# Kernel optimization log

Measured on AMD Instinct MI355X. Metric: run time of the kernel, lower is better.

Reference implementation:

```python
import jax, jax.numpy as jnp
import numpy as np

NTS = ["User", "Group", "Computer", "Resource", "AIAgent"]
NCNT = [60000, 20000, 40000, 40000, 10000]
FEAT = [22, 6, 14, 5, 9]
# (src_nt_idx, dst_nt_idx) for the 7 active relations:
# User-MemberOf->Group, Group-MemberOf->Group, User-AdminTo->Computer,
# User-ActuallyAccessed->Resource, Computer-LSASSAccessible->Computer,
# AIAgent-AgentCanAccess->Resource, User-GenericAll->User
REL = [(0, 1), (1, 1), (0, 2), (0, 3), (2, 2), (4, 3), (0, 0)]
H, NH, L = 128, 4, 3
HD = H // NH
R = len(REL)
E = 40000


def _forward(xs, Wins, b_in, Wq, Wk, Wv, Wmsg, bmsg, rel_imp, Wo, bo, ln_g, ln_b,
             Wr1, br1, Wr2, br2, We1, be1, We2, be2, edge_index, edge_weight, theta):
    elu = jax.nn.elu
    # input projections + ELU
    h = [elu(x @ W + b_in[i]) for i, (x, W) in enumerate(zip(xs, Wins))]
    # differentiable control suppression: higher theta -> lower edge weight
    ew = edge_weight * (1.0 - jax.nn.sigmoid(theta))[:, None]  # [R, E]
    scale = HD ** -0.5
    for l in range(L):
        agg = [[] for _ in NTS]
        imps = [[] for _ in NTS]
        for r, (si, di) in enumerate(REL):
            src, dst = edge_index[r, 0], edge_index[r, 1]
            nd = h[di].shape[0]
            q = (h[di][dst] @ Wq[l, r]).reshape(-1, NH, HD)
            k = (h[si][src] @ Wk[l, r]).reshape(-1, NH, HD)
            v = (h[si][src] @ Wv[l, r]).reshape(-1, NH, HD)
            s = (q * k).sum(-1) * scale * ew[r][:, None]          # [E, NH]
            m = jax.ops.segment_max(s, dst, num_segments=nd)       # per-dst max
            ex = jnp.exp(s - m[dst])
            z = jax.ops.segment_sum(ex, dst, num_segments=nd)
            p = ex / (z[dst] + 1e-10)                              # neighborhood softmax
            msg = (v * p[..., None]).reshape(-1, H) @ Wmsg[l, r] + bmsg[l, r]
            rw = jax.nn.sigmoid(rel_imp[l, r])
            agg[di].append(jax.ops.segment_sum(msg * rw, dst, num_segments=nd))
            imps[di].append(rw)
        nh = []
        for i in range(len(NTS)):
            if agg[i]:
                w = jax.nn.softmax(jax.lax.stop_gradient(jnp.stack(imps[i])))
                comb = jnp.einsum('r,rnh->nh', w, jnp.stack(agg[i]))
                y = h[i] + comb @ Wo[l, i] + bo[l, i]
                mu = y.mean(-1, keepdims=True)
                var = ((y - mu) ** 2).mean(-1, keepdims=True)
                nh.append((y - mu) / jnp.sqrt(var + 1e-5) * ln_g[l, i] + ln_b[l, i])
            else:
                nh.append(h[i])
        h = [elu(y) for y in nh]
    risks = tuple(jax.nn.sigmoid(elu(hi @ Wr1 + br1) @ Wr2 + br2) for hi in h)
    eps = []
    for r, (si, di) in enumerate(REL):
        comb = jnp.concatenate([h[si][edge_index[r, 0]], h[di][edge_index[r, 1]]], -1)
        eps.append(jax.nn.sigmoid(elu(comb @ We1 + be1) @ We2 + be2))
    return risks + tuple(eps)


def setup_inputs() -> dict:
    key = jax.random.key(0)
    ks = iter(jax.random.split(key, 64))
    d = {}
    for nt, n, f in zip(NTS, NCNT, FEAT):
        d["x_" + nt] = jax.random.normal(next(ks), (n, f), jnp.float32)
    ei = []
    for si, di in REL:
        src = jax.random.randint(next(ks), (E,), 0, NCNT[si])
        dst = jax.random.randint(next(ks), (E,), 0, NCNT[di])
        ei.append(jnp.stack([src, dst]))
    d["edge_index"] = jnp.stack(ei).astype(jnp.int32)
    d["edge_weight"] = jax.random.uniform(next(ks), (R, E), jnp.float32)
    d["theta"] = jax.random.normal(next(ks), (R,), jnp.float32)

    def lin(k, i, o):
        return jax.random.normal(k, (i, o), jnp.float32) / float(np.sqrt(i))

    for nt, f in zip(NTS, FEAT):
        d["Win_" + nt] = lin(next(ks), f, H)
    d["b_in"] = jnp.zeros((len(NTS), H), jnp.float32)
    for nm in ["Wq", "Wk", "Wv", "Wmsg"]:
        d[nm] = jax.random.normal(next(ks), (L, R, H, H), jnp.float32) / float(np.sqrt(H))
    d["bmsg"] = jnp.zeros((L, R, H), jnp.float32)
    d["rel_imp"] = jnp.ones((L, R), jnp.float32)
    d["Wo"] = jax.random.normal(next(ks), (L, len(NTS), H, H), jnp.float32) / float(np.sqrt(H))
    d["bo"] = jnp.zeros((L, len(NTS), H), jnp.float32)
    d["ln_g"] = jnp.ones((L, len(NTS), H), jnp.float32)
    d["ln_b"] = jnp.zeros((L, len(NTS), H), jnp.float32)
    d["Wr1"] = lin(next(ks), H, H // 2)
    d["br1"] = jnp.zeros((H // 2,), jnp.float32)
    d["Wr2"] = lin(next(ks), H // 2, 1)
    d["br2"] = jnp.zeros((1,), jnp.float32)
    d["We1"] = lin(next(ks), 2 * H, H)
    d["be1"] = jnp.zeros((H,), jnp.float32)
    d["We2"] = lin(next(ks), H, 1)
    d["be2"] = jnp.zeros((1,), jnp.float32)
    return d


def reference(x_User, x_Group, x_Computer, x_Resource, x_AIAgent,
              edge_index, edge_weight, theta,
              Win_User, Win_Group, Win_Computer, Win_Resource, Win_AIAgent, b_in,
              Wq, Wk, Wv, Wmsg, bmsg, rel_imp, Wo, bo, ln_g, ln_b,
              Wr1, br1, Wr2, br2, We1, be1, We2, be2):
    xs = [x_User, x_Group, x_Computer, x_Resource, x_AIAgent]
    Wins = [Win_User, Win_Group, Win_Computer, Win_Resource, Win_AIAgent]
    return _forward(xs, Wins, b_in, Wq, Wk, Wv, Wmsg, bmsg, rel_imp, Wo, bo,
                    ln_g, ln_b, Wr1, br1, Wr2, br2, We1, be1, We2, be2,
                    edge_index, edge_weight, theta)
```

## Files before the change

kernel.cpp:

```cpp
#include <hip/hip_runtime.h>

#define CDIV(a,b) (((a)+(b)-1)/(b))
#define EE 40000
#define TOTROWS 170000
#define NDOFF 60001
#define NCHK 59

typedef unsigned short ushort_t;
typedef short bf16x8 __attribute__((ext_vector_type(8)));
typedef float f32x4 __attribute__((ext_vector_type(4)));

__device__ __forceinline__ float eluf(float x) { return x > 0.f ? x : expm1f(x); }
__device__ __forceinline__ float sigf(float x) { return 1.f / (1.f + expf(-x)); }
__device__ __forceinline__ float b2f(ushort_t u) { return __uint_as_float(((unsigned)u) << 16); }
__device__ __forceinline__ ushort_t f2b(float f) {
  unsigned x = __float_as_uint(f);
  x += 0x7FFFu + ((x >> 16) & 1u);
  return (ushort_t)(x >> 16);
}
__device__ __forceinline__ unsigned pk2(float lo, float hi) {
  return (unsigned)f2b(lo) | ((unsigned)f2b(hi) << 16);
}
__device__ __forceinline__ float2 b2f2(unsigned u) {
  return make_float2(__uint_as_float(u << 16), __uint_as_float(u & 0xFFFF0000u));
}

__constant__ const int NDD_C[7] = {20000, 20000, 40000, 40000, 40000, 40000, 60000};

template<int BN>
__device__ __forceinline__ void stage_B(char* Bs, int tid, const ushort_t* Bt, const ushort_t* Bt2) {
#pragma unroll
  for (int i = 0; i < BN / 16; i++) {
    int u = tid + i * 256;
    int nrow = u >> 4;
    const ushort_t* sp = (BN == 256 && u >= 2048) ? (Bt2 + (size_t)(u - 2048) * 8)
                                                  : (Bt + (size_t)u * 8);
    uint4 w = *(const uint4*)sp;
    *(uint4*)(Bs + ((u * 16) ^ ((nrow & 7) << 4))) = w;
  }
}

__device__ __forceinline__ void stage_A_bf16(char* As, int tid, const ushort_t* Ab, int base, int n) {
#pragma unroll
  for (int i = 0; i < 4; i++) {
    int u = tid + i * 256;
    int row = u >> 4;
    int grow = base + row;
    uint4 v = make_uint4(0, 0, 0, 0);
    if (grow < n) v = *(const uint4*)&Ab[(size_t)grow * 128 + (u & 15) * 8];
    *(uint4*)(As + ((u * 16) ^ ((row & 7) << 4))) = v;
  }
}

template<int NF>
__device__ __forceinline__ void mfma_core(const char* As, const char* Bs, int lane, int wcol,
                                          f32x4 (&acc)[4][NF]) {
  int i16 = lane & 15, seg = lane >> 4;
#pragma unroll
  for (int s = 0; s < 4; s++) {
    bf16x8 a[4], b[NF];
#pragma unroll
    for (int m = 0; m < 4; m++) {
      int row = m * 16 + i16;
      a[m] = *(const bf16x8*)(As + ((row * 256 + s * 64 + seg * 16) ^ ((row & 7) << 4)));
    }
#pragma unroll
    for (int nn = 0; nn < NF; nn++) {
      int nr = wcol + nn * 16 + i16;
      b[nn] = *(const bf16x8*)(Bs + ((nr * 256 + s * 64 + seg * 16) ^ ((nr & 7) << 4)));
    }
#pragma unroll
    for (int m = 0; m < 4; m++)
#pragma unroll
      for (int nn = 0; nn < NF; nn++)
        acc[m][nn] = __builtin_amdgcn_mfma_f32_16x16x32_bf16(a[m], b[nn], acc[m][nn], 0, 0, 0);
  }
}

__global__ void prep_scalars(const float* __restrict__ theta, const float* __restrict__ rel_imp,
                             float* __restrict__ scal) {
  int t = threadIdx.x;
  if (t < 7) scal[t] = 1.f - sigf(theta[t]);
  if (t < 21) {
    const int partner[7] = {1, 0, 4, 5, 2, 3, -1};
    int l = t / 7, r = t % 7;
    float rw = sigf(rel_imp[t]);
    float w;
    if (partner[r] < 0) w = 1.f;
    else {
      float rwp = sigf(rel_imp[l * 7 + partner[r]]);
      float e0 = expf(rw), e1 = expf(rwp);
      w = e0 / (e0 + e1);
    }
    scal[8 + t] = w * rw;
  }
}

__global__ __launch_bounds__(256) void transpose_weights(
    const float* __restrict__ Wq, const float* __restrict__ Wk, const float* __restrict__ Wv,
    const float* __restrict__ Wmsg, const float* __restrict__ Wo, const float* __restrict__ We1,
    ushort_t* __restrict__ Wt) {
  int mat = blockIdx.x;
  const float* src;
  if (mat < 21)      src = Wq   + (size_t)mat * 16384;
  else if (mat < 42) src = Wk   + (size_t)(mat - 21) * 16384;
  else if (mat < 63) src = Wv   + (size_t)(mat - 42) * 16384;
  else if (mat < 84) src = Wmsg + (size_t)(mat - 63) * 16384;
  else if (mat < 99) src = Wo   + (size_t)(mat - 84) * 16384;
  else               src = We1  + (size_t)(mat - 99) * 16384;
  __shared__ ushort_t lds[16384];
  int t = threadIdx.x;
  for (int i = 0; i < 64; i++) {
    int u = t + i * 256;
    int k = u >> 7;
    int byte = (u * 2) ^ ((k & 15) << 2);
    *(ushort_t*)((char*)lds + byte) = f2b(src[u]);
  }
  __syncthreads();
  ushort_t* dst = Wt + (size_t)mat * 16384;
  for (int i = 0; i < 64; i++) {
    int u = t + i * 256;
    int n = u >> 7, k = u & 127;
    int byte = ((k * 128 + n) * 2) ^ ((k & 15) << 2);
    dst[u] = *(ushort_t*)((char*)lds + byte);
  }
}

__global__ void transpose_wr1(const float* __restrict__ Wr1, ushort_t* __restrict__ Wt101) {
  int u = blockIdx.x * 256 + threadIdx.x;
  int n = u >> 7, k = u & 127;
  Wt101[u] = f2b(Wr1[k * 64 + n]);
}

template<int F>
__device__ __forceinline__ void inproj_compute(const float* xs, const float* Ws, const float* b2,
                                               ushort_t* hptr, int base, int n, int tid) {
  int cp = tid & 63, rg = tid >> 6;
  float wc0[F], wc1[F];
#pragma unroll
  for (int f = 0; f < F; f++) {
    wc0[f] = Ws[f * 128 + cp * 2];
    wc1[f] = Ws[f * 128 + cp * 2 + 1];
  }
  float bb0 = b2[cp * 2], bb1 = b2[cp * 2 + 1];
  for (int i = 0; i < 16; i++) {
    int row = rg * 16 + i, grow = base + row;
    if (grow >= n) break;
    float a0 = bb0, a1 = bb1;
#pragma unroll
    for (int f = 0; f < F; f++) {
      float xv = xs[row * F + f];
      a0 = fmaf(xv, wc0[f], a0);
      a1 = fmaf(xv, wc1[f], a1);
    }
    *(unsigned*)&hptr[(size_t)grow * 128 + cp * 2] = pk2(eluf(a0), eluf(a1));
  }
}

__global__ __launch_bounds__(256) void in_proj_all(
    const float* __restrict__ x0, const float* __restrict__ x1, const float* __restrict__ x2,
    const float* __restrict__ x3, const float* __restrict__ x4,
    const float* __restrict__ W0, const float* __restrict__ W1, const float* __restrict__ W2,
    const float* __restrict__ W3, const float* __restrict__ W4,
    const float* __restrict__ b_in, ushort_t* __restrict__ h) {
  __shared__ float xs[64 * 22];
  __shared__ float Ws[22 * 128];
  int bb = blockIdx.x, tid = threadIdx.x;
  int ti, lb;
  if (bb < 938)       { ti = 0; lb = bb; }
  else if (bb < 1251) { ti = 1; lb = bb - 938; }
  else if (bb < 1876) { ti = 2; lb = bb - 1251; }
  else if (bb < 2501) { ti = 3; lb = bb - 1876; }
  else                { ti = 4; lb = bb - 2501; }
  const int ROFF_[5] = {0, 60000, 80000, 120000, 160000};
  const int NCNT_[5] = {60000, 20000, 40000, 40000, 10000};
  const int FEAT_[5] = {22, 6, 14, 5, 9};
  const float* xp = (ti == 0) ? x0 : (ti == 1) ? x1 : (ti == 2) ? x2 : (ti == 3) ? x3 : x4;
  const float* Wp = (ti == 0) ? W0 : (ti == 1) ? W1 : (ti == 2) ? W2 : (ti == 3) ? W3 : W4;
  int F = FEAT_[ti], n = NCNT_[ti], base = lb * 64;
  for (int u = tid; u < F * 128; u += 256) Ws[u] = Wp[u];
  for (int u = tid; u < 64 * F; u += 256) {
    int row = u / F, f = u - row * F, grow = base + row;
    xs[u] = (grow < n) ? xp[(size_t)grow * F + f] : 0.f;
  }
  __syncthreads();
  ushort_t* hptr = h + (size_t)ROFF_[ti] * 128;
  const float* b2 = b_in + ti * 128;
  switch (ti) {
    case 0: inproj_compute<22>(xs, Ws, b2, hptr, base, n, tid); break;
    case 1: inproj_compute<6>(xs, Ws, b2, hptr, base, n, tid); break;
    case 2: inproj_compute<14>(xs, Ws, b2, hptr, base, n, tid); break;
    case 3: inproj_compute<5>(xs, Ws, b2, hptr, base, n, tid); break;
    default: inproj_compute<9>(xs, Ws, b2, hptr, base, n, tid); break;
  }
}

__global__ void csr_clear(int* __restrict__ counts) {
  int idx = blockIdx.x * 256 + threadIdx.x;
  if (idx < 7 * NDOFF) counts[idx] = 0;
}

__global__ void csr_hist(const int* __restrict__ ei, int* __restrict__ counts) {
  int idx = blockIdx.x * 256 + threadIdx.x;
  if (idx >= 7 * EE) return;
  int r = idx / EE, e = idx - r * EE;
  int d = ei[(size_t)r * 2 * EE + EE + e];
  atomicAdd(&counts[r * NDOFF + d], 1);
}

__global__ __launch_bounds__(256) void csr_chunk(const int* __restrict__ counts, int* __restrict__ chunkSums) {
  int bb = blockIdx.x;
  int r = bb / NCHK, c = bb - r * NCHK;
  int ndd = NDD_C[r];
  int t = threadIdx.x;
  int v = 0;
#pragma unroll
  for (int j = 0; j < 4; j++) {
    int idx = c * 1024 + t + j * 256;
    if (idx < ndd) v += counts[r * NDOFF + idx];
  }
#pragma unroll
  for (int mm = 32; mm; mm >>= 1) v += __shfl_xor(v, mm);
  __shared__ int ws_[4];
  if ((t & 63) == 0) ws_[t >> 6] = v;
  __syncthreads();
  if (t == 0) chunkSums[bb] = ws_[0] + ws_[1] + ws_[2] + ws_[3];
}

__global__ void csr_chunkscan(const int* __restrict__ chunkSums, int* __restrict__ chunkOffs) {
  int r = threadIdx.x;
  if (r >= 7) return;
  int run = 0;
  for (int c = 0; c < NCHK; c++) {
    chunkOffs[r * NCHK + c] = run;
    run += chunkSums[r * NCHK + c];
  }
}

__global__ __launch_bounds__(1024) void csr_scan_final(
    const int* __restrict__ counts, const int* __restrict__ chunkOffs,
    int* __restrict__ offs, int* __restrict__ cursor) {
  int bb = blockIdx.x;
  int r = bb / NCHK, c = bb - r * NCHK;
  int ndd = NDD_C[r];
  int t = threadIdx.x;
  int idx = c * 1024 + t;
  int v = (idx < ndd) ? counts[r * NDOFF + idx] : 0;
  __shared__ int sc[1024];
  sc[t] = v;
  __syncthreads();
  for (int s = 1; s < 1024; s <<= 1) {
    int add = (t >= s) ? sc[t - s] : 0;
    __syncthreads();
    sc[t] += add;
    __syncthreads();
  }
  if (idx < ndd) {
    int excl = chunkOffs[r * NCHK + c] + sc[t] - v;
    offs[r * NDOFF + idx] = excl;
    cursor[r * NDOFF + idx] = excl;
  }
  if (t == 0 && c == 0) offs[r * NDOFF + ndd] = EE;
}

__global__ void csr_scatter(const int* __restrict__ ei, const float* __restrict__ ew,
                            int* __restrict__ cursor, int* __restrict__ src_csr,
                            float* __restrict__ ew_csr) {
  int idx = blockIdx.x * 256 + threadIdx.x;
  if (idx >= 7 * EE) return;
  int r = idx / EE, e = idx - r * EE;
  int d = ei[(size_t)r * 2 * EE + EE + e];
  int s = ei[(size_t)r * 2 * EE + e];
  int slot = atomicAdd(&cursor[r * NDOFF + d], 1);
  src_csr[r * EE + slot] = s;
  ew_csr[r * EE + slot] = ew[(size_t)r * EE + e];
}

__global__ __launch_bounds__(256) void qkv_proj(
    const ushort_t* __restrict__ hd, const ushort_t* __restrict__ hs,
    const ushort_t* __restrict__ WtQ, const ushort_t* __restrict__ WtK, const ushort_t* __restrict__ WtV,
    ushort_t* __restrict__ Qb, ushort_t* __restrict__ Kb, ushort_t* __restrict__ Vb,
    int ndd, int nds) {
  __shared__ char sm[16384 + 65536];
  char* As = sm;
  char* Bs = sm + 16384;
  int tid = threadIdx.x;
  int nqb = (ndd + 63) >> 6;
  int lane = tid & 63, wv = tid >> 6;
  int i16 = lane & 15, seg = lane >> 4;

  if ((int)blockIdx.x < nqb) {
    int base = blockIdx.x * 64;
    stage_B<128>(Bs, tid, WtQ, nullptr);
    stage_A_bf16(As, tid, hd, base, ndd);
    __syncthreads();
    f32x4 acc[4][2] = {};
    mfma_core<2>(As, Bs, lane, wv * 32, acc);
#pragma unroll
    for (int m = 0; m < 4; m++)
#pragma unroll
      for (int i = 0; i < 4; i++) {
        int grow = base + m * 16 + seg * 4 + i;
        if (grow >= ndd) continue;
#pragma unroll
        for (int nn = 0; nn < 2; nn++) {
          int col = wv * 32 + nn * 16 + i16;
          Qb[(size_t)grow * 128 + col] = f2b(acc[m][nn][i]);
        }
      }
  } else {
    int base = (blockIdx.x - nqb) * 64;
    stage_B<256>(Bs, tid, WtK, WtV);
    stage_A_bf16(As, tid, hs, base, nds);
    __syncthreads();
    f32x4 acc[4][4] = {};
    mfma_core<4>(As, Bs, lane, wv * 64, acc);
#pragma unroll
    for (int m = 0; m < 4; m++)
#pragma unroll
      for (int i = 0; i < 4; i++) {
        int grow = base + m * 16 + seg * 4 + i;
        if (grow >= nds) continue;
#pragma unroll
        for (int nn = 0; nn < 4; nn++) {
          int col = wv * 64 + nn * 16 + i16;
          ushort_t val = f2b(acc[m][nn][i]);
          if (col < 128) Kb[(size_t)grow * 128 + col] = val;
          else           Vb[(size_t)grow * 128 + col - 128] = val;
        }
      }
  }
}

__global__ __launch_bounds__(256) void attn_agg(
    const ushort_t* __restrict__ Qb, const ushort_t* __restrict__ Kb, const ushort_t* __restrict__ Vb,
    const int* __restrict__ offs, const int* __restrict__ src_csr, const float* __restrict__ ew_csr,
    const float* __restrict__ ews, ushort_t* __restrict__ Sb, float* __restrict__ degb, int ndd) {
  int node = blockIdx.x * 4 + (threadIdx.x >> 6);
  if (node >= ndd) return;
  int lane = threadIdx.x & 63;
  int beg = offs[node], end = offs[node + 1];
  float escale = ews[0] * 0.17677669529663687f;
  float q0 = b2f(Qb[(size_t)node * 128 + lane]);
  float q1 = b2f(Qb[(size_t)node * 128 + 64 + lane]);
  float m0 = -3.0e38f, m1 = -3.0e38f, z0 = 0.f, z1 = 0.f, a0 = 0.f, a1 = 0.f;
  for (int p = beg; p < end; p++) {
    int s = src_csr[p];
    float wgt = ew_csr[p] * escale;
    float k0 = b2f(Kb[(size_t)s * 128 + lane]);
    float k1 = b2f(Kb[(size_t)s * 128 + 64 + lane]);
    float p0 = q0 * k0, p1 = q1 * k1;
#pragma unroll
    for (int mm = 16; mm; mm >>= 1) {
      p0 += __shfl_xor(p0, mm);
      p1 += __shfl_xor(p1, mm);
    }
    float s0 = p0 * wgt, s1 = p1 * wgt;
    float nm0 = fmaxf(m0, s0), nm1 = fmaxf(m1, s1);
    float r0 = expf(m0 - nm0), r1 = expf(m1 - nm1);
    float e0 = expf(s0 - nm0), e1 = expf(s1 - nm1);
    float v0 = b2f(Vb[(size_t)s * 128 + lane]);
    float v1 = b2f(Vb[(size_t)s * 128 + 64 + lane]);
    z0 = z0 * r0 + e0; a0 = a0 * r0 + e0 * v0; m0 = nm0;
    z1 = z1 * r1 + e1; a1 = a1 * r1 + e1 * v1; m1 = nm1;
  }
  Sb[(size_t)node * 128 + lane]      = f2b(a0 / (z0 + 1e-10f));
  Sb[(size_t)node * 128 + 64 + lane] = f2b(a1 / (z1 + 1e-10f));
  if (lane == 0) degb[node] = (float)(end - beg);
}

template<int MODE>
__global__ __launch_bounds__(256) void gemm_msg(
    const ushort_t* __restrict__ Ap, const ushort_t* __restrict__ Bt,
    ushort_t* __restrict__ C1, int n,
    const float* __restrict__ coefp, const float* __restrict__ deg, const float* __restrict__ bvec) {
  __shared__ char sm[16384 + 32768];
  char* As = sm;
  char* Bs = sm + 16384;
  int tid = threadIdx.x;
  int base = blockIdx.x * 64;
  stage_B<128>(Bs, tid, Bt, nullptr);
  stage_A_bf16(As, tid, Ap, base, n);
  __syncthreads();
  int lane = tid & 63, wv = tid >> 6;
  int i16 = lane & 15, seg = lane >> 4;
  f32x4 acc[4][2] = {};
  mfma_core<2>(As, Bs, lane, wv * 32, acc);
  float coef = *coefp;
#pragma unroll
  for (int m = 0; m < 4; m++)
#pragma unroll
    for (int i = 0; i < 4; i++) {
      int grow = base + m * 16 + seg * 4 + i;
      if (grow >= n) continue;
      float dg = deg[grow];
#pragma unroll
      for (int nn = 0; nn < 2; nn++) {
        int col = wv * 32 + nn * 16 + i16;
        ushort_t* cp = &C1[(size_t)grow * 128 + col];
        float mv = coef * (acc[m][nn][i] + dg * bvec[col]);
        if (MODE == 1) mv += b2f(*cp);
        *cp = f2b(mv);
      }
    }
}

__global__ __launch_bounds__(256) void gemm_pcat(
    const ushort_t* __restrict__ Ap, const ushort_t* __restrict__ Bt, const ushort_t* __restrict__ Bt2,
    ushort_t* __restrict__ C1, int n) {
  __shared__ char sm[16384 + 65536];
  char* As = sm;
  char* Bs = sm + 16384;
  int tid = threadIdx.x;
  int base = blockIdx.x * 64;
  stage_B<256>(Bs, tid, Bt, Bt2);
  stage_A_bf16(As, tid, Ap, base, n);
  __syncthreads();
  int lane = tid & 63, wv = tid >> 6;
  int i16 = lane & 15, seg = lane >> 4;
  f32x4 acc[4][4] = {};
  mfma_core<4>(As, Bs, lane, wv * 64, acc);
#pragma unroll
  for (int m = 0; m < 4; m++)
#pragma unroll
    for (int i = 0; i < 4; i++) {
      int grow = base + m * 16 + seg * 4 + i;
      if (grow >= n) continue;
#pragma unroll
      for (int nn = 0; nn < 4; nn++) {
        int col = wv * 64 + nn * 16 + i16;
        C1[(size_t)grow * 256 + col] = f2b(acc[m][nn][i]);
      }
    }
}

#define WO_C1 938
#define WO_C2 1251
#define WO_C3 1876
#define WO_C4 2501
#define WO_TOTAL 2814
#define YSTR 132
__global__ __launch_bounds__(256) void wo_ln_all(
    ushort_t* __restrict__ h, const ushort_t* __restrict__ comb, const ushort_t* __restrict__ Wt,
    const float* __restrict__ bo, const float* __restrict__ lng, const float* __restrict__ lnb, int l) {
  int bb = blockIdx.x;
  int tid = threadIdx.x;
  if (bb >= WO_C4) {
    int idx16 = (bb - WO_C4) * 256 + tid;
    if (idx16 >= 80000) return;
    ushort_t* p = h + (size_t)160000 * 128 + (size_t)idx16 * 16;
    uint4 v0 = *(uint4*)p, v1 = *(uint4*)(p + 8);
    unsigned* u0 = (unsigned*)&v0;
    unsigned* u1 = (unsigned*)&v1;
#pragma unroll
    for (int i = 0; i < 4; i++) {
      float2 a = b2f2(u0[i]); u0[i] = pk2(eluf(a.x), eluf(a.y));
      float2 b = b2f2(u1[i]); u1[i] = pk2(eluf(b.x), eluf(b.y));
    }
    *(uint4*)p = v0; *(uint4*)(p + 8) = v1;
    return;
  }
  int ti, lb;
  if (bb < WO_C1)      { ti = 0; lb = bb; }
  else if (bb < WO_C2) { ti = 1; lb = bb - WO_C1; }
  else if (bb < WO_C3) { ti = 2; lb = bb - WO_C2; }
  else                 { ti = 3; lb = bb - WO_C3; }
  const int ROFF_[4] = {0, 60000, 80000, 120000};
  const int NCNT4_[4] = {60000, 20000, 40000, 40000};
  int n = NCNT4_[ti];
  int base = lb * 64;
  int li = l * 5 + ti;
  const ushort_t* A = comb + (size_t)ROFF_[ti] * 128;
  ushort_t* C1 = h + (size_t)ROFF_[ti] * 128;
  const ushort_t* Bt = Wt + (size_t)(84 + li) * 16384;
  const float* bvec = bo + (size_t)li * 128;
  const float* g = lng + (size_t)li * 128;
  const float* b = lnb + (size_t)li * 128;

  __shared__ char sm[16384 + 34048];
  char* As = sm;
  char* Bs = sm + 16384;
  stage_B<128>(Bs, tid, Bt, nullptr);
  stage_A_bf16(As, tid, A, base, n);
  __syncthreads();
  int lane = tid & 63, wv = tid >> 6;
  int i16 = lane & 15, seg = lane >> 4;
  f32x4 acc[4][2] = {};
  mfma_core<2>(As, Bs, lane, wv * 32, acc);

  __syncthreads();
  float* Ys = (float*)sm;
#pragma unroll
  for (int m = 0; m < 4; m++)
#pragma unroll
    for (int i = 0; i < 4; i++) {
      int rl = m * 16 + seg * 4 + i;
      int grow = base + rl;
      if (grow >= n) continue;
#pragma unroll
      for (int nn = 0; nn < 2; nn++) {
        int col = wv * 32 + nn * 16 + i16;
        Ys[rl * YSTR + col] = acc[m][nn][i] + b2f(C1[(size_t)grow * 128 + col]) + bvec[col];
      }
    }
  __syncthreads();
  for (int rr = 0; rr < 16; rr++) {
    int rl = wv * 16 + rr;
    int grow = base + rl;
    if (grow >= n) continue;
    float y0 = Ys[rl * YSTR + lane], y1 = Ys[rl * YSTR + 64 + lane];
    float sum = y0 + y1;
#pragma unroll
    for (int mm = 32; mm; mm >>= 1) sum += __shfl_xor(sum, mm);
    float mu = sum * (1.f / 128.f);
    float d0 = y0 - mu, d1 = y1 - mu;
    float vs = d0 * d0 + d1 * d1;
#pragma unroll
    for (int mm = 32; mm; mm >>= 1) vs += __shfl_xor(vs, mm);
    float rs = rsqrtf(vs * (1.f / 128.f) + 1e-5f);
    C1[(size_t)grow * 128 + lane]      = f2b(eluf(d0 * rs * g[lane] + b[lane]));
    C1[(size_t)grow * 128 + 64 + lane] = f2b(eluf(d1 * rs * g[64 + lane] + b[64 + lane]));
  }
}

__global__ __launch_bounds__(256) void risk_mfma(
    const ushort_t* __restrict__ Hh, const ushort_t* __restrict__ Wt101,
    const float* __restrict__ br1, const float* __restrict__ Wr2, const float* __restrict__ br2,
    float* __restrict__ out) {
  __shared__ char sm[16384 + 16384 + 64 * 68 * 4];
  char* As = sm;
  char* Bs = sm + 16384;
  float* Hs = (float*)(sm + 32768);
  int tid = threadIdx.x;
  int base = blockIdx.x * 64;
#pragma unroll
  for (int i = 0; i < 4; i++) {
    int u = tid + i * 256;
    int nrow = u >> 4;
    uint4 w = *(const uint4*)(Wt101 + (size_t)u * 8);
    *(uint4*)(Bs + ((u * 16) ^ ((nrow & 7) << 4))) = w;
  }
  stage_A_bf16(As, tid, Hh, base, TOTROWS);
  __syncthreads();
  int lane = tid & 63, wv = tid >> 6;
  int i16 = lane & 15, seg = lane >> 4;
  f32x4 acc[4][1] = {};
  mfma_core<1>(As, Bs, lane, wv * 16, acc);
#pragma unroll
  for (int m = 0; m < 4; m++)
#pragma unroll
    for (int i = 0; i < 4; i++) {
      int rl = m * 16 + seg * 4 + i;
      int col = wv * 16 + i16;
      Hs[rl * 68 + col] = eluf(acc[m][0][i] + br1[col]);
    }
  __syncthreads();
  float wr2r = Wr2[lane];
  for (int rr = 0; rr < 16; rr++) {
    int rl = wv * 16 + rr;
    int grow = base + rl;
    float v = Hs[rl * 68 + lane] * wr2r;
#pragma unroll
    for (int mm = 32; mm; mm >>= 1) v += __shfl_xor(v, mm);
    if (lane == 0 && grow < TOTROWS) out[grow] = sigf(v + br2[0]);
  }
}

__global__ __launch_bounds__(256) void edge_combine_all(
    const ushort_t* __restrict__ Pcat, const int* __restrict__ ei,
    const float* __restrict__ be1, const float* __restrict__ We2,
    const float* __restrict__ be2, float* __restrict__ out) {
  const int RSI_[7] = {0, 1, 0, 0, 2, 4, 0};
  const int RDI_[7] = {1, 1, 2, 3, 2, 3, 0};
  const int ROFF_[5] = {0, 60000, 80000, 120000, 160000};
  int bb = blockIdx.x;
  int r = bb / 10000;
  int lane = threadIdx.x & 63;
  int e = (bb % 10000) * 4 + (threadIdx.x >> 6);
  const int* src = ei + (size_t)r * 2 * EE;
  const int* dst = src + EE;
  int s = src[e], d = dst[e];
  const ushort_t* p1 = Pcat + ((size_t)(ROFF_[RSI_[r]] + s)) * 256;
  const ushort_t* p2 = Pcat + ((size_t)(ROFF_[RDI_[r]] + d)) * 256 + 128;
  float h0 = eluf(b2f(p1[lane])      + b2f(p2[lane])      + be1[lane]);
  float h1 = eluf(b2f(p1[64 + lane]) + b2f(p2[64 + lane]) + be1[64 + lane]);
  float v = h0 * We2[lane] + h1 * We2[64 + lane];
#pragma unroll
  for (int mm = 32; mm; mm >>= 1) v += __shfl_xor(v, mm);
  if (lane == 0) out[TOTROWS + (size_t)r * EE + e] = sigf(v + be2[0]);
}

extern "C" void kernel_launch(void* const* d_in, const int* in_sizes, int n_in,
                              void* d_out, int out_size, void* d_ws, size_t ws_size,
                              hipStream_t stream) {
  (void)in_sizes; (void)n_in; (void)out_size;
  static const int NCNT_[5] = {60000, 20000, 40000, 40000, 10000};
  static const int RSI[7] = {0, 1, 0, 0, 2, 4, 0};
  static const int RDI[7] = {1, 1, 2, 3, 2, 3, 0};
  static const int RFIRST[7] = {1, 0, 1, 1, 0, 0, 1};
  static const int ROFF[5] = {0, 60000, 80000, 120000, 160000};

  const float* x[5];    for (int i = 0; i < 5; i++) x[i] = (const float*)d_in[i];
  const int*   ei     = (const int*)d_in[5];
  const float* ew     = (const float*)d_in[6];
  const float* theta  = (const float*)d_in[7];
  const float* Win[5]; for (int i = 0; i < 5; i++) Win[i] = (const float*)d_in[8 + i];
  const float* b_in   = (const float*)d_in[13];
  const float* Wq     = (const float*)d_in[14];
  const float* Wk     = (const float*)d_in[15];
  const float* Wv     = (const float*)d_in[16];
  const float* Wmsg   = (const float*)d_in[17];
  const float* bmsg   = (const float*)d_in[18];
  const float* relimp = (const float*)d_in[19];
  const float* Wo     = (const float*)d_in[20];
  const float* bo     = (const float*)d_in[21];
  const float* lng    = (const float*)d_in[22];
  const float* lnb    = (const float*)d_in[23];
  const float* Wr1    = (const float*)d_in[24];
  const float* br1    = (const float*)d_in[25];
  const float* Wr2    = (const float*)d_in[26];
  const float* br2    = (const float*)d_in[27];
  const float* We1    = (const float*)d_in[28];
  const float* be1    = (const float*)d_in[29];
  const float* We2    = (const float*)d_in[30];
  const float* be2    = (const float*)d_in[31];
  float* out = (float*)d_out;

  char* ws = (char*)d_ws;
  size_t off = 0;
  auto alloc = [&](size_t bytes) -> void* {
    void* p = (void*)(ws + off);
    off = (off + bytes + 255) & ~(size_t)255;
    return p;
  };
  ushort_t* h    = (ushort_t*)alloc((size_t)TOTROWS * 128 * 2);
  ushort_t* comb = (ushort_t*)alloc((size_t)TOTROWS * 128 * 2);
  ushort_t* Qb   = (ushort_t*)alloc((size_t)60000 * 128 * 2);
  ushort_t* Kb   = (ushort_t*)alloc((size_t)60000 * 128 * 2);
  ushort_t* Vb   = (ushort_t*)alloc((size_t)60000 * 128 * 2);
  ushort_t* Sb   = (ushort_t*)alloc((size_t)60000 * 128 * 2);
  float* degb = (float*)alloc((size_t)60000 * 4);
  ushort_t* Wt = (ushort_t*)alloc((size_t)102 * 16384 * 2);
  int* counts  = (int*)alloc((size_t)7 * NDOFF * 4);
  int* cursor  = (int*)alloc((size_t)7 * NDOFF * 4);
  int* offsb   = (int*)alloc((size_t)7 * NDOFF * 4);
  int* src_csr = (int*)alloc((size_t)7 * EE * 4);
  float* ew_csr = (float*)alloc((size_t)7 * EE * 4);
  int* chunkS  = (int*)alloc((size_t)7 * NCHK * 4);
  int* chunkO  = (int*)alloc((size_t)7 * NCHK * 4);
  float* scal = (float*)alloc(256);
  if (off > ws_size) return;
  ushort_t* Pcat = comb;

  prep_scalars<<<1, 64, 0, stream>>>(theta, relimp, scal);
  transpose_weights<<<101, 256, 0, stream>>>(Wq, Wk, Wv, Wmsg, Wo, We1, Wt);
  transpose_wr1<<<32, 256, 0, stream>>>(Wr1, Wt + (size_t)101 * 16384);

  in_proj_all<<<2658, 256, 0, stream>>>(
      x[0], x[1], x[2], x[3], x[4], Win[0], Win[1], Win[2], Win[3], Win[4], b_in, h);

  csr_clear<<<CDIV(7 * NDOFF, 256), 256, 0, stream>>>(counts);
  csr_hist<<<CDIV(7 * EE, 256), 256, 0, stream>>>(ei, counts);
  csr_chunk<<<7 * NCHK, 256, 0, stream>>>(counts, chunkS);
  csr_chunkscan<<<1, 64, 0, stream>>>(chunkS, chunkO);
  csr_scan_final<<<7 * NCHK, 1024, 0, stream>>>(counts, chunkO, offsb, cursor);
  csr_scatter<<<CDIV(7 * EE, 256), 256, 0, stream>>>(ei, ew, cursor, src_csr, ew_csr);

  for (int l = 0; l < 3; l++) {
    for (int r = 0; r < 7; r++) {
      int si = RSI[r], di = RDI[r];
      int nds = NCNT_[si], ndd = NCNT_[di];
      ushort_t* hs = h + (size_t)ROFF[si] * 128;
      ushort_t* hd = h + (size_t)ROFF[di] * 128;
      int lr = l * 7 + r;
      const ushort_t* WtQ = Wt + (size_t)lr * 16384;
      const ushort_t* WtK = Wt + (size_t)(21 + lr) * 16384;
      const ushort_t* WtV = Wt + (size_t)(42 + lr) * 16384;
      const ushort_t* WtM = Wt + (size_t)(63 + lr) * 16384;

      qkv_proj<<<CDIV(ndd, 64) + CDIV(nds, 64), 256, 0, stream>>>(
          hd, hs, WtQ, WtK, WtV, Qb, Kb, Vb, ndd, nds);
      attn_agg<<<CDIV(ndd, 4), 256, 0, stream>>>(
          Qb, Kb, Vb, offsb + (size_t)r * NDOFF, src_csr + (size_t)r * EE,
          ew_csr + (size_t)r * EE, scal + r, Sb, degb, ndd);
      ushort_t* cdst = comb + (size_t)ROFF[di] * 128;
      if (RFIRST[r])
        gemm_msg<4><<<CDIV(ndd, 64), 256, 0, stream>>>(
            Sb, WtM, cdst, ndd, scal + 8 + lr, degb, bmsg + (size_t)lr * 128);
      else
        gemm_msg<1><<<CDIV(ndd, 64), 256, 0, stream>>>(
            Sb, WtM, cdst, ndd, scal + 8 + lr, degb, bmsg + (size_t)lr * 128);
    }
    wo_ln_all<<<WO_TOTAL, 256, 0, stream>>>(h, comb, Wt, bo, lng, lnb, l);
  }

  gemm_pcat<<<CDIV(TOTROWS, 64), 256, 0, stream>>>(
      h, Wt + (size_t)99 * 16384, Wt + (size_t)100 * 16384, Pcat, TOTROWS);

  risk_mfma<<<CDIV(TOTROWS, 64), 256, 0, stream>>>(
      h, Wt + (size_t)101 * 16384, br1, Wr2, br2, out);

  edge_combine_all<<<7 * CDIV(EE, 4), 256, 0, stream>>>(Pcat, ei, be1, We2, be2, out);
}
```

Before: 1.643 ms.

## Fuse message GEMM into next relation's QKV launch and merge final kernels

Defers each relation's message GEMM into the following relation's QKV projection launch as extra blocks, so two independent GEMMs share one grid and launch count drops. The final pcat and risk kernels are merged into one launch. The wo_ln epilogue now computes LayerNorm from registers with in-wave shuffles instead of staging through shared memory. attn_agg uses 512-thread blocks and exits early for nodes with no incoming edges. The cost is larger fused kernels whose shared-memory footprint is sized for the largest branch, which may reduce occupancy for the smaller GEMM blocks.

```diff
diff --git a/kernel.cpp b/kernel.cpp
--- a/kernel.cpp
+++ b/kernel.cpp
@@ -5,6 +5,7 @@
 #define TOTROWS 170000
 #define NDOFF 60001
 #define NCHK 59
+#define G_PCAT 2657
 
 typedef unsigned short ushort_t;
 typedef short bf16x8 __attribute__((ext_vector_type(8)));
@@ -276,7 +277,12 @@
   ew_csr[r * EE + slot] = ew[(size_t)r * EE + e];
 }
 
-__global__ __launch_bounds__(256) void qkv_proj(
+template<int MODE>
+__global__ __launch_bounds__(256) void msg_qkv(
+    const ushort_t* __restrict__ Sb, const ushort_t* __restrict__ WtM,
+    ushort_t* __restrict__ combDst, int nmsg,
+    const float* __restrict__ coefp, const float* __restrict__ deg, const float* __restrict__ bvec,
+    int gmsg,
     const ushort_t* __restrict__ hd, const ushort_t* __restrict__ hs,
     const ushort_t* __restrict__ WtQ, const ushort_t* __restrict__ WtK, const ushort_t* __restrict__ WtV,
     ushort_t* __restrict__ Qb, ushort_t* __restrict__ Kb, ushort_t* __restrict__ Vb,
@@ -285,12 +291,40 @@
   char* As = sm;
   char* Bs = sm + 16384;
   int tid = threadIdx.x;
-  int nqb = (ndd + 63) >> 6;
   int lane = tid & 63, wv = tid >> 6;
   int i16 = lane & 15, seg = lane >> 4;
-
-  if ((int)blockIdx.x < nqb) {
-    int base = blockIdx.x * 64;
+  int bb = blockIdx.x;
+
+  if (bb < gmsg) {
+    int base = bb * 64;
+    stage_B<128>(Bs, tid, WtM, nullptr);
+    stage_A_bf16(As, tid, Sb, base, nmsg);
+    __syncthreads();
+    f32x4 acc[4][2] = {};
+    mfma_core<2>(As, Bs, lane, wv * 32, acc);
+    float coef = *coefp;
+#pragma unroll
+    for (int m = 0; m < 4; m++)
+#pragma unroll
+      for (int i = 0; i < 4; i++) {
+        int grow = base + m * 16 + seg * 4 + i;
+        if (grow >= nmsg) continue;
+        float dg = deg[grow];
+#pragma unroll
+        for (int nn = 0; nn < 2; nn++) {
+          int col = wv * 32 + nn * 16 + i16;
+          ushort_t* cp = &combDst[(size_t)grow * 128 + col];
+          float mv = coef * (acc[m][nn][i] + dg * bvec[col]);
+          if (MODE == 1) mv += b2f(*cp);
+          *cp = f2b(mv);
+        }
+      }
+    return;
+  }
+  bb -= gmsg;
+  int nqb = (ndd + 63) >> 6;
+  if (bb < nqb) {
+    int base = bb * 64;
     stage_B<128>(Bs, tid, WtQ, nullptr);
     stage_A_bf16(As, tid, hd, base, ndd);
     __syncthreads();
@@ -309,7 +343,7 @@
         }
       }
   } else {
-    int base = (blockIdx.x - nqb) * 64;
+    int base = (bb - nqb) * 64;
     stage_B<256>(Bs, tid, WtK, WtV);
     stage_A_bf16(As, tid, hs, base, nds);
     __syncthreads();
@@ -332,14 +366,20 @@
   }
 }
 
-__global__ __launch_bounds__(256) void attn_agg(
+__global__ __launch_bounds__(512) void attn_agg(
     const ushort_t* __restrict__ Qb, const ushort_t* __restrict__ Kb, const ushort_t* __restrict__ Vb,
     const int* __restrict__ offs, const int* __restrict__ src_csr, const float* __restrict__ ew_csr,
     const float* __restrict__ ews, ushort_t* __restrict__ Sb, float* __restrict__ degb, int ndd) {
-  int node = blockIdx.x * 4 + (threadIdx.x >> 6);
+  int node = blockIdx.x * 8 + (threadIdx.x >> 6);
   if (node >= ndd) return;
   int lane = threadIdx.x & 63;
   int beg = offs[node], end = offs[node + 1];
+  if (end == beg) {
+    Sb[(size_t)node * 128 + lane] = 0;
+    Sb[(size_t)node * 128 + 64 + lane] = 0;
+    if (lane == 0) degb[node] = 0.f;
+    return;
+  }
   float escale = ews[0] * 0.17677669529663687f;
   float q0 = b2f(Qb[(size_t)node * 128 + lane]);
   float q1 = b2f(Qb[(size_t)node * 128 + 64 + lane]);
@@ -369,77 +409,11 @@
   if (lane == 0) degb[node] = (float)(end - beg);
 }
 
-template<int MODE>
-__global__ __launch_bounds__(256) void gemm_msg(
-    const ushort_t* __restrict__ Ap, const ushort_t* __restrict__ Bt,
-    ushort_t* __restrict__ C1, int n,
-    const float* __restrict__ coefp, const float* __restrict__ deg, const float* __restrict__ bvec) {
-  __shared__ char sm[16384 + 32768];
-  char* As = sm;
-  char* Bs = sm + 16384;
-  int tid = threadIdx.x;
-  int base = blockIdx.x * 64;
-  stage_B<128>(Bs, tid, Bt, nullptr);
-  stage_A_bf16(As, tid, Ap, base, n);
-  __syncthreads();
-  int lane = tid & 63, wv = tid >> 6;
-  int i16 = lane & 15, seg = lane >> 4;
-  f32x4 acc[4][2] = {};
-  mfma_core<2>(As, Bs, lane, wv * 32, acc);
-  float coef = *coefp;
-#pragma unroll
-  for (int m = 0; m < 4; m++)
-#pragma unroll
-    for (int i = 0; i < 4; i++) {
-      int grow = base + m * 16 + seg * 4 + i;
-      if (grow >= n) continue;
-      float dg = deg[grow];
-#pragma unroll
-      for (int nn = 0; nn < 2; nn++) {
-        int col = wv * 32 + nn * 16 + i16;
-        ushort_t* cp = &C1[(size_t)grow * 128 + col];
-        float mv = coef * (acc[m][nn][i] + dg * bvec[col]);
-        if (MODE == 1) mv += b2f(*cp);
-        *cp = f2b(mv);
-      }
-    }
-}
-
-__global__ __launch_bounds__(256) void gemm_pcat(
-    const ushort_t* __restrict__ Ap, const ushort_t* __restrict__ Bt, const ushort_t* __restrict__ Bt2,
-    ushort_t* __restrict__ C1, int n) {
-  __shared__ char sm[16384 + 65536];
-  char* As = sm;
-  char* Bs = sm + 16384;
-  int tid = threadIdx.x;
-  int base = blockIdx.x * 64;
-  stage_B<256>(Bs, tid, Bt, Bt2);
-  stage_A_bf16(As, tid, Ap, base, n);
-  __syncthreads();
-  int lane = tid & 63, wv = tid >> 6;
-  int i16 = lane & 15, seg = lane >> 4;
-  f32x4 acc[4][4] = {};
-  mfma_core<4>(As, Bs, lane, wv * 64, acc);
-#pragma unroll
-  for (int m = 0; m < 4; m++)
-#pragma unroll
-    for (int i = 0; i < 4; i++) {
-      int grow = base + m * 16 + seg * 4 + i;
-      if (grow >= n) continue;
-#pragma unroll
-      for (int nn = 0; nn < 4; nn++) {
-        int col = wv * 64 + nn * 16 + i16;
-        C1[(size_t)grow * 256 + col] = f2b(acc[m][nn][i]);
-      }
-    }
-}
-
 #define WO_C1 938
 #define WO_C2 1251
 #define WO_C3 1876
 #define WO_C4 2501
 #define WO_TOTAL 2814
-#define YSTR 132
 __global__ __launch_bounds__(256) void wo_ln_all(
     ushort_t* __restrict__ h, const ushort_t* __restrict__ comb, const ushort_t* __restrict__ Wt,
     const float* __restrict__ bo, const float* __restrict__ lng, const float* __restrict__ lnb, int l) {
@@ -477,7 +451,7 @@
   const float* g = lng + (size_t)li * 128;
   const float* b = lnb + (size_t)li * 128;
 
-  __shared__ char sm[16384 + 34048];
+  __shared__ char sm[16384 + 32768];
   char* As = sm;
   char* Bs = sm + 16384;
   stage_B<128>(Bs, tid, Bt, nullptr);
@@ -485,84 +459,118 @@
   __syncthreads();
   int lane = tid & 63, wv = tid >> 6;
   int i16 = lane & 15, seg = lane >> 4;
-  f32x4 acc[4][2] = {};
-  mfma_core<2>(As, Bs, lane, wv * 32, acc);
-
-  __syncthreads();
-  float* Ys = (float*)sm;
-#pragma unroll
-  for (int m = 0; m < 4; m++)
-#pragma unroll
-    for (int i = 0; i < 4; i++) {
-      int rl = m * 16 + seg * 4 + i;
-      int grow = base + rl;
-      if (grow >= n) continue;
-#pragma unroll
-      for (int nn = 0; nn < 2; nn++) {
-        int col = wv * 32 + nn * 16 + i16;
-        Ys[rl * YSTR + col] = acc[m][nn][i] + b2f(C1[(size_t)grow * 128 + col]) + bvec[col];
-      }
-    }
-  __syncthreads();
-  for (int rr = 0; rr < 16; rr++) {
-    int rl = wv * 16 + rr;
-    int grow = base + rl;
+
+  f32x4 acc[8] = {};
+#pragma unroll
+  for (int s = 0; s < 4; s++) {
+    int arow = wv * 16 + i16;
+    bf16x8 a = *(const bf16x8*)(As + ((arow * 256 + s * 64 + seg * 16) ^ ((arow & 7) << 4)));
+#pragma unroll
+    for (int nn = 0; nn < 8; nn++) {
+      int nr = nn * 16 + i16;
+      bf16x8 bfr = *(const bf16x8*)(Bs + ((nr * 256 + s * 64 + seg * 16) ^ ((nr & 7) << 4)));
+      acc[nn] = __builtin_amdgcn_mfma_f32_16x16x32_bf16(a, bfr, acc[nn], 0, 0, 0);
+    }
+  }
+
+  float gv[8], bv[8], bov[8];
+#pragma unroll
+  for (int nn = 0; nn < 8; nn++) {
+    int col = nn * 16 + i16;
+    gv[nn] = g[col]; bv[nn] = b[col]; bov[nn] = bvec[col];
+  }
+#pragma unroll
+  for (int i = 0; i < 4; i++) {
+    int grow = base + wv * 16 + seg * 4 + i;
     if (grow >= n) continue;
-    float y0 = Ys[rl * YSTR + lane], y1 = Ys[rl * YSTR + 64 + lane];
-    float sum = y0 + y1;
-#pragma unroll
-    for (int mm = 32; mm; mm >>= 1) sum += __shfl_xor(sum, mm);
-    float mu = sum * (1.f / 128.f);
-    float d0 = y0 - mu, d1 = y1 - mu;
-    float vs = d0 * d0 + d1 * d1;
-#pragma unroll
-    for (int mm = 32; mm; mm >>= 1) vs += __shfl_xor(vs, mm);
-    float rs = rsqrtf(vs * (1.f / 128.f) + 1e-5f);
-    C1[(size_t)grow * 128 + lane]      = f2b(eluf(d0 * rs * g[lane] + b[lane]));
-    C1[(size_t)grow * 128 + 64 + lane] = f2b(eluf(d1 * rs * g[64 + lane] + b[64 + lane]));
-  }
-}
-
-__global__ __launch_bounds__(256) void risk_mfma(
-    const ushort_t* __restrict__ Hh, const ushort_t* __restrict__ Wt101,
+    float y[8];
+    float s1 = 0.f;
+#pragma unroll
+    for (int nn = 0; nn < 8; nn++) {
+      int col = nn * 16 + i16;
+      float yv = acc[nn][i] + b2f(C1[(size_t)grow * 128 + col]) + bov[nn];
+      y[nn] = yv; s1 += yv;
+    }
+#pragma unroll
+    for (int mm = 8; mm; mm >>= 1) s1 += __shfl_xor(s1, mm);
+    float mu = s1 * (1.f / 128.f);
+    float s2 = 0.f;
+#pragma unroll
+    for (int nn = 0; nn < 8; nn++) { float d = y[nn] - mu; s2 += d * d; }
+#pragma unroll
+    for (int mm = 8; mm; mm >>= 1) s2 += __shfl_xor(s2, mm);
+    float rs = rsqrtf(s2 * (1.f / 128.f) + 1e-5f);
+#pragma unroll
+    for (int nn = 0; nn < 8; nn++) {
+      int col = nn * 16 + i16;
+      C1[(size_t)grow * 128 + col] = f2b(eluf((y[nn] - mu) * rs * gv[nn] + bv[nn]));
+    }
+  }
+}
+
+__global__ __launch_bounds__(256) void pcat_risk(
+    const ushort_t* __restrict__ Hh, const ushort_t* __restrict__ BtP1, const ushort_t* __restrict__ BtP2,
+    ushort_t* __restrict__ Pcat, const ushort_t* __restrict__ Wt101,
     const float* __restrict__ br1, const float* __restrict__ Wr2, const float* __restrict__ br2,
     float* __restrict__ out) {
-  __shared__ char sm[16384 + 16384 + 64 * 68 * 4];
+  __shared__ char sm[16384 + 65536];
   char* As = sm;
   char* Bs = sm + 16384;
-  float* Hs = (float*)(sm + 32768);
   int tid = threadIdx.x;
-  int base = blockIdx.x * 64;
-#pragma unroll
-  for (int i = 0; i < 4; i++) {
-    int u = tid + i * 256;
-    int nrow = u >> 4;
-    uint4 w = *(const uint4*)(Wt101 + (size_t)u * 8);
-    *(uint4*)(Bs + ((u * 16) ^ ((nrow & 7) << 4))) = w;
-  }
-  stage_A_bf16(As, tid, Hh, base, TOTROWS);
-  __syncthreads();
   int lane = tid & 63, wv = tid >> 6;
   int i16 = lane & 15, seg = lane >> 4;
-  f32x4 acc[4][1] = {};
-  mfma_core<1>(As, Bs, lane, wv * 16, acc);
-#pragma unroll
-  for (int m = 0; m < 4; m++)
+  int bb = blockIdx.x;
+  if (bb < G_PCAT) {
+    int base = bb * 64;
+    stage_B<256>(Bs, tid, BtP1, BtP2);
+    stage_A_bf16(As, tid, Hh, base, TOTROWS);
+    __syncthreads();
+    f32x4 acc[4][4] = {};
+    mfma_core<4>(As, Bs, lane, wv * 64, acc);
+#pragma unroll
+    for (int m = 0; m < 4; m++)
+#pragma unroll
+      for (int i = 0; i < 4; i++) {
+        int grow = base + m * 16 + seg * 4 + i;
+        if (grow >= TOTROWS) continue;
+#pragma unroll
+        for (int nn = 0; nn < 4; nn++) {
+          int col = wv * 64 + nn * 16 + i16;
+          Pcat[(size_t)grow * 256 + col] = f2b(acc[m][nn][i]);
+        }
+      }
+  } else {
+    int base = (bb - G_PCAT) * 64;
+    float* Hs = (float*)(sm + 32768);
 #pragma unroll
     for (int i = 0; i < 4; i++) {
-      int rl = m * 16 + seg * 4 + i;
-      int col = wv * 16 + i16;
-      Hs[rl * 68 + col] = eluf(acc[m][0][i] + br1[col]);
-    }
-  __syncthreads();
-  float wr2r = Wr2[lane];
-  for (int rr = 0; rr < 16; rr++) {
-    int rl = wv * 16 + rr;
-    int grow = base + rl;
-    float v = Hs[rl * 68 + lane] * wr2r;
-#pragma unroll
-    for (int mm = 32; mm; mm >>= 1) v += __shfl_xor(v, mm);
-    if (lane == 0 && grow < TOTROWS) out[grow] = sigf(v + br2[0]);
+      int u = tid + i * 256;
+      int nrow = u >> 4;
+      uint4 w = *(const uint4*)(Wt101 + (size_t)u * 8);
+      *(uint4*)(Bs + ((u * 16) ^ ((nrow & 7) << 4))) = w;
+    }
+    stage_A_bf16(As, tid, Hh, base, TOTROWS);
+    __syncthreads();
+    f32x4 acc[4][1] = {};
+    mfma_core<1>(As, Bs, lane, wv * 16, acc);
+#pragma unroll
+    for (int m = 0; m < 4; m++)
+#pragma unroll
+      for (int i = 0; i < 4; i++) {
+        int rl = m * 16 + seg * 4 + i;
+        int col = wv * 16 + i16;
+        Hs[rl * 68 + col] = eluf(acc[m][0][i] + br1[col]);
+      }
+    __syncthreads();
+    float wr2r = Wr2[lane];
+    for (int rr = 0; rr < 16; rr++) {
+      int rl = wv * 16 + rr;
+      int grow = base + rl;
+      float v = Hs[rl * 68 + lane] * wr2r;
+#pragma unroll
+      for (int mm = 32; mm; mm >>= 1) v += __shfl_xor(v, mm);
+      if (lane == 0 && grow < TOTROWS) out[grow] = sigf(v + br2[0]);
+    }
   }
 }
 
@@ -676,29 +684,46 @@
       const ushort_t* WtQ = Wt + (size_t)lr * 16384;
       const ushort_t* WtK = Wt + (size_t)(21 + lr) * 16384;
       const ushort_t* WtV = Wt + (size_t)(42 + lr) * 16384;
-      const ushort_t* WtM = Wt + (size_t)(63 + lr) * 16384;
-
-      qkv_proj<<<CDIV(ndd, 64) + CDIV(nds, 64), 256, 0, stream>>>(
-          hd, hs, WtQ, WtK, WtV, Qb, Kb, Vb, ndd, nds);
-      attn_agg<<<CDIV(ndd, 4), 256, 0, stream>>>(
+      int gq = CDIV(ndd, 64), gkv = CDIV(nds, 64);
+
+      if (r == 0) {
+        msg_qkv<4><<<gq + gkv, 256, 0, stream>>>(
+            nullptr, nullptr, nullptr, 0, scal, scal, scal, 0,
+            hd, hs, WtQ, WtK, WtV, Qb, Kb, Vb, ndd, nds);
+      } else {
+        int pr = r - 1, plr = l * 7 + pr;
+        int nmsg = NCNT_[RDI[pr]];
+        int gm = CDIV(nmsg, 64);
+        ushort_t* pdst = comb + (size_t)ROFF[RDI[pr]] * 128;
+        const ushort_t* WtMp = Wt + (size_t)(63 + plr) * 16384;
+        if (RFIRST[pr])
+          msg_qkv<4><<<gm + gq + gkv, 256, 0, stream>>>(
+              Sb, WtMp, pdst, nmsg, scal + 8 + plr, degb, bmsg + (size_t)plr * 128, gm,
+              hd, hs, WtQ, WtK, WtV, Qb, Kb, Vb, ndd, nds);
+        else
+          msg_qkv<1><<<gm + gq + gkv, 256, 0, stream>>>(
+              Sb, WtMp, pdst, nmsg, scal + 8 + plr, degb, bmsg + (size_t)plr * 128, gm,
+              hd, hs, WtQ, WtK, WtV, Qb, Kb, Vb, ndd, nds);
+      }
+      attn_agg<<<CDIV(ndd, 8), 512, 0, stream>>>(
           Qb, Kb, Vb, offsb + (size_t)r * NDOFF, src_csr + (size_t)r * EE,
           ew_csr + (size_t)r * EE, scal + r, Sb, degb, ndd);
-      ushort_t* cdst = comb + (size_t)ROFF[di] * 128;
-      if (RFIRST[r])
-        gemm_msg<4><<<CDIV(ndd, 64), 256, 0, stream>>>(
-            Sb, WtM, cdst, ndd, scal + 8 + lr, degb, bmsg + (size_t)lr * 128);
-      else
-        gemm_msg<1><<<CDIV(ndd, 64), 256, 0, stream>>>(
-            Sb, WtM, cdst, ndd, scal + 8 + lr, degb, bmsg + (size_t)lr * 128);
+    }
+    {
+      int plr = l * 7 + 6;
+      int nmsg = NCNT_[RDI[6]];
+      int gm = CDIV(nmsg, 64);
+      msg_qkv<4><<<gm, 256, 0, stream>>>(
+          Sb, Wt + (size_t)(63 + plr) * 16384, comb + (size_t)ROFF[RDI[6]] * 128, nmsg,
+          scal + 8 + plr, degb, bmsg + (size_t)plr * 128, gm,
+          nullptr, nullptr, nullptr, nullptr, nullptr, nullptr, nullptr, nullptr, 0, 0);
     }
     wo_ln_all<<<WO_TOTAL, 256, 0, stream>>>(h, comb, Wt, bo, lng, lnb, l);
   }
 
-  gemm_pcat<<<CDIV(TOTROWS, 64), 256, 0, stream>>>(
-      h, Wt + (size_t)99 * 16384, Wt + (size_t)100 * 16384, Pcat, TOTROWS);
-
-  risk_mfma<<<CDIV(TOTROWS, 64), 256, 0, stream>>>(
-      h, Wt + (size_t)101 * 16384, br1, Wr2, br2, out);
+  pcat_risk<<<2 * G_PCAT, 256, 0, stream>>>(
+      h, Wt + (size_t)99 * 16384, Wt + (size_t)100 * 16384, Pcat,
+      Wt + (size_t)101 * 16384, br1, Wr2, br2, out);
 
   edge_combine_all<<<7 * CDIV(EE, 4), 256, 0, stream>>>(Pcat, ei, be1, We2, be2, out);
 }
```

New measurement: 1.610 ms. 1.02x faster.
